# Performance work log

Hardware: AMD Instinct MI355X
Metric: run time of the kernel (lower is better)

## Reference

```python
import jax, jax.numpy as jnp
import numpy as np

SLOPE = 25.0  # snntorch surrogate.fast_sigmoid default slope

@jax.custom_vjp
def fast_sigmoid(x):
    # Forward: Heaviside step (spike); backward: fast-sigmoid surrogate grad.
    return (x > 0).astype(x.dtype)

def _fs_fwd(x):
    return fast_sigmoid(x), x

def _fs_bwd(x, g):
    return (g / (SLOPE * jnp.abs(x) + 1.0) ** 2,)

fast_sigmoid.defvjp(_fs_fwd, _fs_bwd)


def setup_inputs() -> dict:
    key = jax.random.key(0)
    k0, k1, k2, k3, k4 = jax.random.split(key, 5)
    B, IN, OUT, T = 512, 512, 512, 64
    x = jax.random.normal(k0, (B, IN), jnp.float32)
    W = jax.random.normal(k1, (OUT, IN), jnp.float32) / np.sqrt(IN).astype(np.float32)
    b = jnp.zeros((OUT,), jnp.float32)
    # learnable scalars (0.0 in source init; small nonzero to exercise the P recurrence)
    alpha = jax.random.uniform(k2, (1,), jnp.float32) * 0.1
    eta = jax.random.uniform(k3, (1,), jnp.float32) * 0.01
    beta = jax.random.uniform(k4, (1,), jnp.float32) * 0.1
    P0 = jnp.zeros((OUT, IN), jnp.float32)
    return {"x": x, "W": W, "b": b, "alpha": alpha, "eta": eta, "beta": beta, "P0": P0, "T": T}


def reference(x, W, b, alpha, eta, beta, P0, T):
    # x: [B, IN], W: [OUT, IN], P0: [OUT, IN]
    tao_u, tao_w, dt, V_th = 5.0, 1.0, 1.0, 0.2
    k = jnp.float32(dt / tao_u)
    a = alpha.reshape(())
    e = eta.reshape(())
    bt = beta.reshape(())
    # MLP output is constant across timesteps (same s_batch each step)
    mlp_T = jax.nn.relu(x @ W.T + b).T  # [OUT, B]
    xT = x.T  # [IN, B]
    decay_p = jnp.exp(jnp.float32(-dt / tao_w))

    # NOTE: reset() zeroes u and s every step, so only P is recurrent:
    # u_m = k * (mlp_out * exp(-m/tao_w) + alpha * P @ x^T)
    def step(P, m):
        u = k * (mlp_T * jnp.exp(-m / tao_w) + a * (P @ xT))  # [OUT, B]
        P_new = P * decay_p + e * ((fast_sigmoid(u) + bt) @ x)  # [OUT, IN]
        s = fast_sigmoid(u - V_th)  # [OUT, B]
        return P_new, s.T  # emit [B, OUT]

    _, spk = jax.lax.scan(step, P0, jnp.arange(T, dtype=jnp.float32))
    return spk  # [T, B, OUT]
```

## Files before the change

### kernel.cpp

```cpp
#include <hip/hip_runtime.h>


#define NN 512

__global__ __launch_bounds__(256) void gemm64_kernel(
    const float* __restrict__ x, const float* __restrict__ W,
    const float* __restrict__ P0, const float* __restrict__ bias,
    float* __restrict__ M, float* __restrict__ V0, float* __restrict__ G)
{
    const int tid = threadIdx.x;
    const int bid = blockIdx.x;
    const int out = bid >> 6;
    const int tl = bid & 63;
    const int rb = (tl >> 3) << 6;
    const int cb = (tl & 7) << 6;

    const float* A = ((out == 0) ? W : (out == 1) ? P0 : x) + (size_t)rb * NN;
    const float* Bx = x + (size_t)cb * NN;
    float* D = (out == 0) ? M : (out == 1) ? V0 : G;

    const int tx = tid & 15;
    const int ty = tid >> 4;

    __shared__ float At[32][68];
    __shared__ float Bt[32][68];

    const int lr = tid >> 2;
    const int lk = (tid & 3) << 3;

    float acc[4][4] = {{0.f,0.f,0.f,0.f},{0.f,0.f,0.f,0.f},
                       {0.f,0.f,0.f,0.f},{0.f,0.f,0.f,0.f}};

    float4 a0 = *(const float4*)(A + (size_t)lr * NN + lk);
    float4 a1 = *(const float4*)(A + (size_t)lr * NN + lk + 4);
    float4 b0 = *(const float4*)(Bx + (size_t)lr * NN + lk);
    float4 b1 = *(const float4*)(Bx + (size_t)lr * NN + lk + 4);

    for (int c = 0; c < 16; ++c) {
        __syncthreads();
        At[lk + 0][lr] = a0.x; At[lk + 1][lr] = a0.y;
        At[lk + 2][lr] = a0.z; At[lk + 3][lr] = a0.w;
        At[lk + 4][lr] = a1.x; At[lk + 5][lr] = a1.y;
        At[lk + 6][lr] = a1.z; At[lk + 7][lr] = a1.w;
        Bt[lk + 0][lr] = b0.x; Bt[lk + 1][lr] = b0.y;
        Bt[lk + 2][lr] = b0.z; Bt[lk + 3][lr] = b0.w;
        Bt[lk + 4][lr] = b1.x; Bt[lk + 5][lr] = b1.y;
        Bt[lk + 6][lr] = b1.z; Bt[lk + 7][lr] = b1.w;
        __syncthreads();

        if (c < 15) {
            const int k0 = (c + 1) << 5;
            a0 = *(const float4*)(A + (size_t)lr * NN + k0 + lk);
            a1 = *(const float4*)(A + (size_t)lr * NN + k0 + lk + 4);
            b0 = *(const float4*)(Bx + (size_t)lr * NN + k0 + lk);
            b1 = *(const float4*)(Bx + (size_t)lr * NN + k0 + lk + 4);
        }

#pragma unroll
        for (int k = 0; k < 32; ++k) {
            const float4 av = *(const float4*)&At[k][4 * ty];
            const float4 bv = *(const float4*)&Bt[k][4 * tx];
            const float avs[4] = {av.x, av.y, av.z, av.w};
            const float bvs[4] = {bv.x, bv.y, bv.z, bv.w};
#pragma unroll
            for (int i = 0; i < 4; ++i)
#pragma unroll
                for (int j = 0; j < 4; ++j)
                    acc[i][j] = fmaf(avs[i], bvs[j], acc[i][j]);
        }
    }

#pragma unroll
    for (int i = 0; i < 4; ++i) {
        const int r = rb + 4 * ty + i;
        float4 o = make_float4(acc[i][0], acc[i][1], acc[i][2], acc[i][3]);
        if (out == 0) {
            const float bb = bias[r];
            o.x = fmaxf(o.x + bb, 0.f); o.y = fmaxf(o.y + bb, 0.f);
            o.z = fmaxf(o.z + bb, 0.f); o.w = fmaxf(o.w + bb, 0.f);
        }
        *(float4*)(D + (size_t)r * NN + cb + 4 * tx) = o;
    }
}

__global__ __launch_bounds__(256) void acc0_kernel(
    const float* __restrict__ M, const float* __restrict__ V0,
    const float* __restrict__ G, const float* __restrict__ alpha,
    float* __restrict__ ACC0)
{
    const int tid = threadIdx.x;
    const int rb = (blockIdx.x >> 4) << 5;
    const int cb = (blockIdx.x & 15) << 5;
    const float a = alpha[0];
    const float kk = 0.2f;

    __shared__ float Ht[32][36];
    __shared__ float Bt[32][36];

    const int tx = tid & 15;
    const int ty = tid >> 4;
    const int lr = tid >> 3;
    const int lk = (tid & 7) << 2;

    float acc[2][2] = {{0.f, 0.f}, {0.f, 0.f}};

    for (int k0 = 0; k0 < NN; k0 += 32) {
        const float4 mv = *(const float4*)(M + (size_t)(rb + lr) * NN + k0 + lk);
        const float4 vv = *(const float4*)(V0 + (size_t)(rb + lr) * NN + k0 + lk);
        const float4 gv = *(const float4*)(G + (size_t)(k0 + lr) * NN + cb + lk);
        __syncthreads();
        Ht[lk + 0][lr] = (kk * fmaf(a, vv.x, mv.x) > 0.f) ? 1.f : 0.f;
        Ht[lk + 1][lr] = (kk * fmaf(a, vv.y, mv.y) > 0.f) ? 1.f : 0.f;
        Ht[lk + 2][lr] = (kk * fmaf(a, vv.z, mv.z) > 0.f) ? 1.f : 0.f;
        Ht[lk + 3][lr] = (kk * fmaf(a, vv.w, mv.w) > 0.f) ? 1.f : 0.f;
        Bt[lr][lk + 0] = gv.x; Bt[lr][lk + 1] = gv.y;
        Bt[lr][lk + 2] = gv.z; Bt[lr][lk + 3] = gv.w;
        __syncthreads();

#pragma unroll
        for (int k = 0; k < 32; ++k) {
            const float2 av = *(const float2*)&Ht[k][2 * ty];
            const float2 bv = *(const float2*)&Bt[k][2 * tx];
            acc[0][0] = fmaf(av.x, bv.x, acc[0][0]);
            acc[0][1] = fmaf(av.x, bv.y, acc[0][1]);
            acc[1][0] = fmaf(av.y, bv.x, acc[1][0]);
            acc[1][1] = fmaf(av.y, bv.y, acc[1][1]);
        }
    }

#pragma unroll
    for (int i = 0; i < 2; ++i) {
        *(float2*)(ACC0 + (size_t)(rb + 2 * ty + i) * NN + cb + 2 * tx) =
            make_float2(acc[i][0], acc[i][1]);
    }
}

__global__ __launch_bounds__(256) void colsum_kernel(
    const float* __restrict__ G, float* __restrict__ gs)
{
    __shared__ float red[4][64];
    const int tid = threadIdx.x;
    const int c = (blockIdx.x << 6) + (tid & 63);
    const int g = tid >> 6;
    float s = 0.f;
#pragma unroll 8
    for (int bp = 128 * g; bp < 128 * g + 128; ++bp) s += G[(size_t)bp * NN + c];
    if (g > 0) red[g][tid & 63] = s;
    __syncthreads();
    if (g == 0) gs[c] = ((s + red[1][tid & 63]) + red[2][tid & 63]) + red[3][tid & 63];
}

__global__ __launch_bounds__(512, 4) void snn_bits7_kernel(
    const float* __restrict__ M, const float* __restrict__ G,
    const float* __restrict__ V0, const float* __restrict__ ACC0,
    const float* __restrict__ gs, const float* __restrict__ alpha,
    const float* __restrict__ eta, const float* __restrict__ beta,
    unsigned* __restrict__ sp, int T)
{
    const int tid = threadIdx.x;
    const int w = tid >> 6;
    const int lane = tid & 63;
    const int r = blockIdx.x;

    __shared__ unsigned long long lflag[2];
    __shared__ int wcnt[8];
    __shared__ unsigned short list[528] __attribute__((aligned(16)));

    const float a = alpha[0], e = eta[0], bt = beta[0];
    const float kk = 0.2f;
    const float dd = 0.36787944117144233f;
    const float Vth = 0.2f;

    const size_t rc = (size_t)r * NN + tid;
    const float m = M[rc];
    float v = V0[rc];
    const float cg = e * bt * gs[tid];
    const float* Gc = G + tid;

    float acc;
    float em;
    unsigned long long oldw;

    {
        const float u = kk * fmaf(a, v, m * 1.0f);
        const unsigned long long hb = __ballot(u > 0.f);
        const unsigned long long sb = __ballot(u > Vth);
        if (lane == 0)
            *(unsigned long long*)(sp + (size_t)r * 16 + 2 * w) = sb;
        oldw = hb;
        acc = ACC0[rc];
        v = fmaf(dd, v, fmaf(e, acc, cg));
        em = dd;
    }

    for (int t = 1; t < T; ++t) {
        const float u = kk * fmaf(a, v, m * em);
        const unsigned long long hb = __ballot(u > 0.f);
        const unsigned long long sb = __ballot(u > Vth);
        const unsigned long long xw = hb ^ oldw;
        const int p = t & 1;
        if (lane == 0) {
            ((unsigned char*)&lflag[p])[w] = (xw != 0ull) ? (unsigned char)1 : (unsigned char)0;
            wcnt[w] = (int)__popcll(xw);
            *(unsigned long long*)(sp + ((size_t)t * NN + r) * 16 + 2 * w) = sb;
        }
        __syncthreads();

        if (lflag[p] != 0ull) {
            const int c0 = wcnt[0], c1 = wcnt[1], c2 = wcnt[2], c3 = wcnt[3];
            const int c4 = wcnt[4], c5 = wcnt[5], c6 = wcnt[6], c7 = wcnt[7];
            const int ntot = ((c0 + c1) + (c2 + c3)) + ((c4 + c5) + (c6 + c7));
            int base = 0;
            if (w > 0) base += c0;
            if (w > 1) base += c1;
            if (w > 2) base += c2;
            if (w > 3) base += c3;
            if (w > 4) base += c4;
            if (w > 5) base += c5;
            if (w > 6) base += c6;

            if ((xw >> lane) & 1ull) {
                const int pos = (int)__popcll(xw & ((1ull << lane) - 1ull));
                const unsigned row = (unsigned)((w << 6) + lane);
                const unsigned sgn = (unsigned)((hb >> lane) & 1ull) << 15;
                list[base + pos] = (unsigned short)(row | sgn);
            }
            __syncthreads();

            float s0 = 0.f, s1 = 0.f, s2 = 0.f, s3 = 0.f;
            float s4 = 0.f, s5 = 0.f, s6 = 0.f, s7 = 0.f;
            for (int j = 0; j < ntot; j += 8) {
                const uint4 le = *(const uint4*)(list + j);
                const unsigned e0 = le.x & 0xFFFFu, e1 = le.x >> 16;
                const unsigned e2 = le.y & 0xFFFFu, e3 = le.y >> 16;
                const unsigned e4 = le.z & 0xFFFFu, e5 = le.z >> 16;
                const unsigned e6 = le.w & 0xFFFFu, e7 = le.w >> 16;
                const float g0 = Gc[(size_t)(e0 & 511u) << 9];
                const float g1 = Gc[(size_t)(e1 & 511u) << 9];
                const float g2 = Gc[(size_t)(e2 & 511u) << 9];
                const float g3 = Gc[(size_t)(e3 & 511u) << 9];
                const float g4 = Gc[(size_t)(e4 & 511u) << 9];
                const float g5 = Gc[(size_t)(e5 & 511u) << 9];
                const float g6 = Gc[(size_t)(e6 & 511u) << 9];
                const float g7 = Gc[(size_t)(e7 & 511u) << 9];
                s0 += (j + 0 < ntot) ? ((e0 & 0x8000u) ? g0 : -g0) : 0.0f;
                s1 += (j + 1 < ntot) ? ((e1 & 0x8000u) ? g1 : -g1) : 0.0f;
                s2 += (j + 2 < ntot) ? ((e2 & 0x8000u) ? g2 : -g2) : 0.0f;
                s3 += (j + 3 < ntot) ? ((e3 & 0x8000u) ? g3 : -g3) : 0.0f;
                s4 += (j + 4 < ntot) ? ((e4 & 0x8000u) ? g4 : -g4) : 0.0f;
                s5 += (j + 5 < ntot) ? ((e5 & 0x8000u) ? g5 : -g5) : 0.0f;
                s6 += (j + 6 < ntot) ? ((e6 & 0x8000u) ? g6 : -g6) : 0.0f;
                s7 += (j + 7 < ntot) ? ((e7 & 0x8000u) ? g7 : -g7) : 0.0f;
            }
            acc += ((s0 + s1) + (s2 + s3)) + ((s4 + s5) + (s6 + s7));
        }

        oldw = hb;
        v = fmaf(dd, v, fmaf(e, acc, cg));
        em *= dd;
    }
}

__global__ __launch_bounds__(256) void expand_kernel(
    const unsigned* __restrict__ sp, float* __restrict__ out)
{
    const int tid = threadIdx.x;
    const int t = blockIdx.x >> 3;
    const int bt8 = blockIdx.x & 7;

    __shared__ uint2 sh[NN];
    const uint2* spw = (const uint2*)sp;
    sh[tid]       = spw[((size_t)t * NN + tid) * 8 + bt8];
    sh[tid + 256] = spw[((size_t)t * NN + tid + 256) * 8 + bt8];
    __syncthreads();

    const int b = bt8 * 64 + (tid >> 2);
    const int sub = tid & 3;
    const int rw = (tid >> 2) >> 5;
    const int bit = b & 31;
    float* op = out + (size_t)t * (NN * NN) + (size_t)b * NN;

#pragma unroll 4
    for (int i = 0; i < 32; ++i) {
        const int o = sub * 4 + i * 16;
        const uint2 w0 = sh[o];
        const uint2 w1 = sh[o + 1];
        const uint2 w2 = sh[o + 2];
        const uint2 w3 = sh[o + 3];
        float4 f;
        f.x = (float)(((rw ? w0.y : w0.x) >> bit) & 1u);
        f.y = (float)(((rw ? w1.y : w1.x) >> bit) & 1u);
        f.z = (float)(((rw ? w2.y : w2.x) >> bit) & 1u);
        f.w = (float)(((rw ? w3.y : w3.x) >> bit) & 1u);
        *(float4*)(op + o) = f;
    }
}

__global__ __launch_bounds__(256) void snn_step_kernel(
    const float* __restrict__ M, const float* __restrict__ G,
    const float* __restrict__ V0, const float* __restrict__ gs,
    const float* __restrict__ alpha, const float* __restrict__ eta,
    const float* __restrict__ beta, float* __restrict__ out, int T)
{
    const int j = threadIdx.x;
    const int r0 = blockIdx.x * 2;
    const int c0 = 2 * j;
    const float a = alpha[0], e = eta[0], bt = beta[0];
    const float kk = 0.2f, dd = 0.36787944117144233f, Vth = 0.2f;

    float v00 = V0[r0 * NN + c0];
    float v01 = V0[r0 * NN + c0 + 1];
    float v10 = V0[(r0 + 1) * NN + c0];
    float v11 = V0[(r0 + 1) * NN + c0 + 1];
    const float m00 = M[r0 * NN + c0];
    const float m01 = M[r0 * NN + c0 + 1];
    const float m10 = M[(r0 + 1) * NN + c0];
    const float m11 = M[(r0 + 1) * NN + c0 + 1];
    const float gs0 = gs[c0];
    const float gs1 = gs[c0 + 1];

    __shared__ float2 hp[NN];
    float em = 1.0f;
    const float2* Gcol = (const float2*)G + j;

    for (int t = 0; t < T; ++t) {
        const float u00 = kk * (m00 * em + a * v00);
        const float u01 = kk * (m01 * em + a * v01);
        const float u10 = kk * (m10 * em + a * v10);
        const float u11 = kk * (m11 * em + a * v11);

        float* outp = out + (size_t)t * (NN * NN);
        float2 sA = make_float2(u00 > Vth ? 1.f : 0.f, u10 > Vth ? 1.f : 0.f);
        float2 sB = make_float2(u01 > Vth ? 1.f : 0.f, u11 > Vth ? 1.f : 0.f);
        *(float2*)(outp + (size_t)c0 * NN + r0) = sA;
        *(float2*)(outp + (size_t)(c0 + 1) * NN + r0) = sB;

        hp[c0]     = make_float2(u00 > 0.f ? 1.f : 0.f, u10 > 0.f ? 1.f : 0.f);
        hp[c0 + 1] = make_float2(u01 > 0.f ? 1.f : 0.f, u11 > 0.f ? 1.f : 0.f);
        __syncthreads();

        float acc00 = 0.f, acc01 = 0.f, acc10 = 0.f, acc11 = 0.f;
#pragma unroll 8
        for (int bp = 0; bp < NN; ++bp) {
            float2 h = hp[bp];
            float2 g = Gcol[(size_t)bp * 256];
            acc00 = fmaf(h.x, g.x, acc00);
            acc01 = fmaf(h.x, g.y, acc01);
            acc10 = fmaf(h.y, g.x, acc10);
            acc11 = fmaf(h.y, g.y, acc11);
        }

        v00 = dd * v00 + e * (acc00 + bt * gs0);
        v01 = dd * v01 + e * (acc01 + bt * gs1);
        v10 = dd * v10 + e * (acc10 + bt * gs0);
        v11 = dd * v11 + e * (acc11 + bt * gs1);
        em *= dd;
        __syncthreads();
    }
}

extern "C" void kernel_launch(void* const* d_in, const int* in_sizes, int n_in,
                              void* d_out, int out_size, void* d_ws, size_t ws_size,
                              hipStream_t stream)
{
    const float* x     = (const float*)d_in[0];
    const float* W     = (const float*)d_in[1];
    const float* bias  = (const float*)d_in[2];
    const float* alpha = (const float*)d_in[3];
    const float* eta   = (const float*)d_in[4];
    const float* beta  = (const float*)d_in[5];
    const float* P0    = (const float*)d_in[6];
    (void)in_sizes; (void)n_in;

    const int T = out_size / (NN * NN);

    float* ws   = (float*)d_ws;
    float* M    = ws;
    float* V0   = ws + NN * NN;
    float* G    = ws + 2 * NN * NN;
    float* ACC0 = ws + 3 * NN * NN;
    float* gsv  = ws + 4 * NN * NN;
    unsigned* sp = (unsigned*)(gsv + NN);

    const size_t need_main = ((size_t)4 * NN * NN + NN) * 4 + (size_t)T * NN * 16 * 4;

    hipLaunchKernelGGL(gemm64_kernel, dim3(192), dim3(256), 0, stream,
                       x, W, P0, bias, M, V0, G);
    hipLaunchKernelGGL(colsum_kernel, dim3(8), dim3(256), 0, stream, G, gsv);

    if (ws_size >= need_main) {
        hipLaunchKernelGGL(acc0_kernel, dim3(256), dim3(256), 0, stream,
                           M, V0, G, alpha, ACC0);
        hipLaunchKernelGGL(snn_bits7_kernel, dim3(NN), dim3(512), 0, stream,
                           M, G, V0, ACC0, gsv, alpha, eta, beta, sp, T);
        hipLaunchKernelGGL(expand_kernel, dim3(T * 8), dim3(256), 0, stream,
                           sp, (float*)d_out);
    } else {
        hipLaunchKernelGGL(snn_step_kernel, dim3(256), dim3(256), 0, stream,
                           M, G, V0, gsv, alpha, eta, beta, (float*)d_out, T);
    }
}
```

Measured before the change: 131.2 us.

## Split-K the initial GEMMs, fuse column sum into ACC0 kernel, unroll gather by 16

The three 512x512 GEMMs are split four ways along K, going from 192 to 768 blocks so the GPU is better filled. A new combine kernel sums the partials and applies bias and ReLU. The column sum of G moves into the ACC0 kernel to save a launch, and the sparse gather loop in the main SNN kernel now processes 16 list entries per iteration to expose more memory-level parallelism. This costs an extra 12 matrices of workspace and extra global traffic for the partials. The original path is kept as a fallback when workspace is small.

```diff
diff --git a/kernel.cpp b/kernel.cpp
--- a/kernel.cpp
+++ b/kernel.cpp
@@ -3,21 +3,23 @@
 
 #define NN 512
 
-__global__ __launch_bounds__(256) void gemm64_kernel(
+__global__ __launch_bounds__(256) void gemm_splitk_kernel(
     const float* __restrict__ x, const float* __restrict__ W,
-    const float* __restrict__ P0, const float* __restrict__ bias,
-    float* __restrict__ M, float* __restrict__ V0, float* __restrict__ G)
+    const float* __restrict__ P0, float* __restrict__ part)
 {
     const int tid = threadIdx.x;
     const int bid = blockIdx.x;
-    const int out = bid >> 6;
-    const int tl = bid & 63;
+    const int out = bid >> 8;
+    const int rem = bid & 255;
+    const int kq = rem >> 6;
+    const int tl = rem & 63;
     const int rb = (tl >> 3) << 6;
     const int cb = (tl & 7) << 6;
+    const int kbase = kq << 7;
 
     const float* A = ((out == 0) ? W : (out == 1) ? P0 : x) + (size_t)rb * NN;
     const float* Bx = x + (size_t)cb * NN;
-    float* D = (out == 0) ? M : (out == 1) ? V0 : G;
+    float* D = part + (size_t)(out * 4 + kq) * NN * NN;
 
     const int tx = tid & 15;
     const int ty = tid >> 4;
@@ -31,12 +33,12 @@
     float acc[4][4] = {{0.f,0.f,0.f,0.f},{0.f,0.f,0.f,0.f},
                        {0.f,0.f,0.f,0.f},{0.f,0.f,0.f,0.f}};
 
-    float4 a0 = *(const float4*)(A + (size_t)lr * NN + lk);
-    float4 a1 = *(const float4*)(A + (size_t)lr * NN + lk + 4);
-    float4 b0 = *(const float4*)(Bx + (size_t)lr * NN + lk);
-    float4 b1 = *(const float4*)(Bx + (size_t)lr * NN + lk + 4);
-
-    for (int c = 0; c < 16; ++c) {
+    float4 a0 = *(const float4*)(A + (size_t)lr * NN + kbase + lk);
+    float4 a1 = *(const float4*)(A + (size_t)lr * NN + kbase + lk + 4);
+    float4 b0 = *(const float4*)(Bx + (size_t)lr * NN + kbase + lk);
+    float4 b1 = *(const float4*)(Bx + (size_t)lr * NN + kbase + lk + 4);
+
+    for (int c = 0; c < 4; ++c) {
         __syncthreads();
         At[lk + 0][lr] = a0.x; At[lk + 1][lr] = a0.y;
         At[lk + 2][lr] = a0.z; At[lk + 3][lr] = a0.w;
@@ -48,8 +50,8 @@
         Bt[lk + 6][lr] = b1.z; Bt[lk + 7][lr] = b1.w;
         __syncthreads();
 
-        if (c < 15) {
-            const int k0 = (c + 1) << 5;
+        if (c < 3) {
+            const int k0 = kbase + ((c + 1) << 5);
             a0 = *(const float4*)(A + (size_t)lr * NN + k0 + lk);
             a1 = *(const float4*)(A + (size_t)lr * NN + k0 + lk + 4);
             b0 = *(const float4*)(Bx + (size_t)lr * NN + k0 + lk);
@@ -73,20 +75,44 @@
 #pragma unroll
     for (int i = 0; i < 4; ++i) {
         const int r = rb + 4 * ty + i;
-        float4 o = make_float4(acc[i][0], acc[i][1], acc[i][2], acc[i][3]);
-        if (out == 0) {
-            const float bb = bias[r];
-            o.x = fmaxf(o.x + bb, 0.f); o.y = fmaxf(o.y + bb, 0.f);
-            o.z = fmaxf(o.z + bb, 0.f); o.w = fmaxf(o.w + bb, 0.f);
-        }
-        *(float4*)(D + (size_t)r * NN + cb + 4 * tx) = o;
-    }
-}
-
-__global__ __launch_bounds__(256) void acc0_kernel(
+        *(float4*)(D + (size_t)r * NN + cb + 4 * tx) =
+            make_float4(acc[i][0], acc[i][1], acc[i][2], acc[i][3]);
+    }
+}
+
+__global__ __launch_bounds__(256) void combine_kernel(
+    const float* __restrict__ part, const float* __restrict__ bias,
+    float* __restrict__ M, float* __restrict__ V0, float* __restrict__ G)
+{
+    const int idx = blockIdx.x * 256 + threadIdx.x;
+    const int out = idx >> 16;
+    const int io = idx & 65535;
+    const float4* p = (const float4*)(part + (size_t)out * 4 * NN * NN);
+    const float4 p0 = p[io];
+    const float4 p1 = p[io + 65536];
+    const float4 p2 = p[io + 131072];
+    const float4 p3 = p[io + 196608];
+    float4 s;
+    s.x = (p0.x + p1.x) + (p2.x + p3.x);
+    s.y = (p0.y + p1.y) + (p2.y + p3.y);
+    s.z = (p0.z + p1.z) + (p2.z + p3.z);
+    s.w = (p0.w + p1.w) + (p2.w + p3.w);
+    if (out == 0) {
+        const float bb = bias[io >> 7];
+        s.x = fmaxf(s.x + bb, 0.f); s.y = fmaxf(s.y + bb, 0.f);
+        s.z = fmaxf(s.z + bb, 0.f); s.w = fmaxf(s.w + bb, 0.f);
+        ((float4*)M)[io] = s;
+    } else if (out == 1) {
+        ((float4*)V0)[io] = s;
+    } else {
+        ((float4*)G)[io] = s;
+    }
+}
+
+__global__ __launch_bounds__(256) void acc0cs_kernel(
     const float* __restrict__ M, const float* __restrict__ V0,
     const float* __restrict__ G, const float* __restrict__ alpha,
-    float* __restrict__ ACC0)
+    float* __restrict__ ACC0, float* __restrict__ gs)
 {
     const int tid = threadIdx.x;
     const int rb = (blockIdx.x >> 4) << 5;
@@ -133,24 +159,29 @@
         *(float2*)(ACC0 + (size_t)(rb + 2 * ty + i) * NN + cb + 2 * tx) =
             make_float2(acc[i][0], acc[i][1]);
     }
-}
-
-__global__ __launch_bounds__(256) void colsum_kernel(
-    const float* __restrict__ G, float* __restrict__ gs)
-{
-    __shared__ float red[4][64];
-    const int tid = threadIdx.x;
-    const int c = (blockIdx.x << 6) + (tid & 63);
-    const int g = tid >> 6;
-    float s = 0.f;
+
+    if (rb == 0) {
+        __syncthreads();
+        float* red = (float*)Ht;
+        const int c = cb + (tid & 31);
+        const int g = tid >> 5;
+        float s = 0.f;
 #pragma unroll 8
-    for (int bp = 128 * g; bp < 128 * g + 128; ++bp) s += G[(size_t)bp * NN + c];
-    if (g > 0) red[g][tid & 63] = s;
-    __syncthreads();
-    if (g == 0) gs[c] = ((s + red[1][tid & 63]) + red[2][tid & 63]) + red[3][tid & 63];
-}
-
-__global__ __launch_bounds__(512, 4) void snn_bits7_kernel(
+        for (int bp = 64 * g; bp < 64 * g + 64; ++bp)
+            s += G[(size_t)bp * NN + c];
+        red[g * 32 + (tid & 31)] = s;
+        __syncthreads();
+        if (g == 0) {
+            const int cc = tid & 31;
+            const float tot =
+                ((red[cc] + red[32 + cc]) + (red[64 + cc] + red[96 + cc])) +
+                ((red[128 + cc] + red[160 + cc]) + (red[192 + cc] + red[224 + cc]));
+            gs[c] = tot;
+        }
+    }
+}
+
+__global__ __launch_bounds__(512, 4) void snn_bits8_kernel(
     const float* __restrict__ M, const float* __restrict__ G,
     const float* __restrict__ V0, const float* __restrict__ ACC0,
     const float* __restrict__ gs, const float* __restrict__ alpha,
@@ -164,7 +195,7 @@
 
     __shared__ unsigned long long lflag[2];
     __shared__ int wcnt[8];
-    __shared__ unsigned short list[528] __attribute__((aligned(16)));
+    __shared__ unsigned short list[544] __attribute__((aligned(16)));
 
     const float a = alpha[0], e = eta[0], bt = beta[0];
     const float kk = 0.2f;
@@ -229,12 +260,17 @@
 
             float s0 = 0.f, s1 = 0.f, s2 = 0.f, s3 = 0.f;
             float s4 = 0.f, s5 = 0.f, s6 = 0.f, s7 = 0.f;
-            for (int j = 0; j < ntot; j += 8) {
-                const uint4 le = *(const uint4*)(list + j);
-                const unsigned e0 = le.x & 0xFFFFu, e1 = le.x >> 16;
-                const unsigned e2 = le.y & 0xFFFFu, e3 = le.y >> 16;
-                const unsigned e4 = le.z & 0xFFFFu, e5 = le.z >> 16;
-                const unsigned e6 = le.w & 0xFFFFu, e7 = le.w >> 16;
+            for (int j = 0; j < ntot; j += 16) {
+                const uint4 leA = *(const uint4*)(list + j);
+                const uint4 leB = *(const uint4*)(list + j + 8);
+                const unsigned e0 = leA.x & 0xFFFFu,  e1 = leA.x >> 16;
+                const unsigned e2 = leA.y & 0xFFFFu,  e3 = leA.y >> 16;
+                const unsigned e4 = leA.z & 0xFFFFu,  e5 = leA.z >> 16;
+                const unsigned e6 = leA.w & 0xFFFFu,  e7 = leA.w >> 16;
+                const unsigned e8 = leB.x & 0xFFFFu,  e9 = leB.x >> 16;
+                const unsigned ea = leB.y & 0xFFFFu,  eb = leB.y >> 16;
+                const unsigned ec = leB.z & 0xFFFFu,  ed = leB.z >> 16;
+                const unsigned ee = leB.w & 0xFFFFu,  ef = leB.w >> 16;
                 const float g0 = Gc[(size_t)(e0 & 511u) << 9];
                 const float g1 = Gc[(size_t)(e1 & 511u) << 9];
                 const float g2 = Gc[(size_t)(e2 & 511u) << 9];
@@ -243,14 +279,30 @@
                 const float g5 = Gc[(size_t)(e5 & 511u) << 9];
                 const float g6 = Gc[(size_t)(e6 & 511u) << 9];
                 const float g7 = Gc[(size_t)(e7 & 511u) << 9];
-                s0 += (j + 0 < ntot) ? ((e0 & 0x8000u) ? g0 : -g0) : 0.0f;
-                s1 += (j + 1 < ntot) ? ((e1 & 0x8000u) ? g1 : -g1) : 0.0f;
-                s2 += (j + 2 < ntot) ? ((e2 & 0x8000u) ? g2 : -g2) : 0.0f;
-                s3 += (j + 3 < ntot) ? ((e3 & 0x8000u) ? g3 : -g3) : 0.0f;
-                s4 += (j + 4 < ntot) ? ((e4 & 0x8000u) ? g4 : -g4) : 0.0f;
-                s5 += (j + 5 < ntot) ? ((e5 & 0x8000u) ? g5 : -g5) : 0.0f;
-                s6 += (j + 6 < ntot) ? ((e6 & 0x8000u) ? g6 : -g6) : 0.0f;
-                s7 += (j + 7 < ntot) ? ((e7 & 0x8000u) ? g7 : -g7) : 0.0f;
+                const float g8 = Gc[(size_t)(e8 & 511u) << 9];
+                const float g9 = Gc[(size_t)(e9 & 511u) << 9];
+                const float ga = Gc[(size_t)(ea & 511u) << 9];
+                const float gb = Gc[(size_t)(eb & 511u) << 9];
+                const float gc2 = Gc[(size_t)(ec & 511u) << 9];
+                const float gd = Gc[(size_t)(ed & 511u) << 9];
+                const float ge = Gc[(size_t)(ee & 511u) << 9];
+                const float gf = Gc[(size_t)(ef & 511u) << 9];
+                s0 += (j + 0  < ntot) ? ((e0 & 0x8000u) ? g0 : -g0) : 0.0f;
+                s1 += (j + 1  < ntot) ? ((e1 & 0x8000u) ? g1 : -g1) : 0.0f;
+                s2 += (j + 2  < ntot) ? ((e2 & 0x8000u) ? g2 : -g2) : 0.0f;
+                s3 += (j + 3  < ntot) ? ((e3 & 0x8000u) ? g3 : -g3) : 0.0f;
+                s4 += (j + 4  < ntot) ? ((e4 & 0x8000u) ? g4 : -g4) : 0.0f;
+                s5 += (j + 5  < ntot) ? ((e5 & 0x8000u) ? g5 : -g5) : 0.0f;
+                s6 += (j + 6  < ntot) ? ((e6 & 0x8000u) ? g6 : -g6) : 0.0f;
+                s7 += (j + 7  < ntot) ? ((e7 & 0x8000u) ? g7 : -g7) : 0.0f;
+                s0 += (j + 8  < ntot) ? ((e8 & 0x8000u) ? g8 : -g8) : 0.0f;
+                s1 += (j + 9  < ntot) ? ((e9 & 0x8000u) ? g9 : -g9) : 0.0f;
+                s2 += (j + 10 < ntot) ? ((ea & 0x8000u) ? ga : -ga) : 0.0f;
+                s3 += (j + 11 < ntot) ? ((eb & 0x8000u) ? gb : -gb) : 0.0f;
+                s4 += (j + 12 < ntot) ? ((ec & 0x8000u) ? gc2 : -gc2) : 0.0f;
+                s5 += (j + 13 < ntot) ? ((ed & 0x8000u) ? gd : -gd) : 0.0f;
+                s6 += (j + 14 < ntot) ? ((ee & 0x8000u) ? ge : -ge) : 0.0f;
+                s7 += (j + 15 < ntot) ? ((ef & 0x8000u) ? gf : -gf) : 0.0f;
             }
             acc += ((s0 + s1) + (s2 + s3)) + ((s4 + s5) + (s6 + s7));
         }
@@ -296,6 +348,101 @@
     }
 }
 
+__global__ __launch_bounds__(256) void gemm64_kernel(
+    const float* __restrict__ x, const float* __restrict__ W,
+    const float* __restrict__ P0, const float* __restrict__ bias,
+    float* __restrict__ M, float* __restrict__ V0, float* __restrict__ G)
+{
+    const int tid = threadIdx.x;
+    const int bid = blockIdx.x;
+    const int out = bid >> 6;
+    const int tl = bid & 63;
+    const int rb = (tl >> 3) << 6;
+    const int cb = (tl & 7) << 6;
+
+    const float* A = ((out == 0) ? W : (out == 1) ? P0 : x) + (size_t)rb * NN;
+    const float* Bx = x + (size_t)cb * NN;
+    float* D = (out == 0) ? M : (out == 1) ? V0 : G;
+
+    const int tx = tid & 15;
+    const int ty = tid >> 4;
+
+    __shared__ float At[32][68];
+    __shared__ float Bt[32][68];
+
+    const int lr = tid >> 2;
+    const int lk = (tid & 3) << 3;
+
+    float acc[4][4] = {{0.f,0.f,0.f,0.f},{0.f,0.f,0.f,0.f},
+                       {0.f,0.f,0.f,0.f},{0.f,0.f,0.f,0.f}};
+
+    float4 a0 = *(const float4*)(A + (size_t)lr * NN + lk);
+    float4 a1 = *(const float4*)(A + (size_t)lr * NN + lk + 4);
+    float4 b0 = *(const float4*)(Bx + (size_t)lr * NN + lk);
+    float4 b1 = *(const float4*)(Bx + (size_t)lr * NN + lk + 4);
+
+    for (int c = 0; c < 16; ++c) {
+        __syncthreads();
+        At[lk + 0][lr] = a0.x; At[lk + 1][lr] = a0.y;
+        At[lk + 2][lr] = a0.z; At[lk + 3][lr] = a0.w;
+        At[lk + 4][lr] = a1.x; At[lk + 5][lr] = a1.y;
+        At[lk + 6][lr] = a1.z; At[lk + 7][lr] = a1.w;
+        Bt[lk + 0][lr] = b0.x; Bt[lk + 1][lr] = b0.y;
+        Bt[lk + 2][lr] = b0.z; Bt[lk + 3][lr] = b0.w;
+        Bt[lk + 4][lr] = b1.x; Bt[lk + 5][lr] = b1.y;
+        Bt[lk + 6][lr] = b1.z; Bt[lk + 7][lr] = b1.w;
+        __syncthreads();
+
+        if (c < 15) {
+            const int k0 = (c + 1) << 5;
+            a0 = *(const float4*)(A + (size_t)lr * NN + k0 + lk);
+            a1 = *(const float4*)(A + (size_t)lr * NN + k0 + lk + 4);
+            b0 = *(const float4*)(Bx + (size_t)lr * NN + k0 + lk);
+            b1 = *(const float4*)(Bx + (size_t)lr * NN + k0 + lk + 4);
+        }
+
+#pragma unroll
+        for (int k = 0; k < 32; ++k) {
+            const float4 av = *(const float4*)&At[k][4 * ty];
+            const float4 bv = *(const float4*)&Bt[k][4 * tx];
+            const float avs[4] = {av.x, av.y, av.z, av.w};
+            const float bvs[4] = {bv.x, bv.y, bv.z, bv.w};
+#pragma unroll
+            for (int i = 0; i < 4; ++i)
+#pragma unroll
+                for (int j = 0; j < 4; ++j)
+                    acc[i][j] = fmaf(avs[i], bvs[j], acc[i][j]);
+        }
+    }
+
+#pragma unroll
+    for (int i = 0; i < 4; ++i) {
+        const int r = rb + 4 * ty + i;
+        float4 o = make_float4(acc[i][0], acc[i][1], acc[i][2], acc[i][3]);
+        if (out == 0) {
+            const float bb = bias[r];
+            o.x = fmaxf(o.x + bb, 0.f); o.y = fmaxf(o.y + bb, 0.f);
+            o.z = fmaxf(o.z + bb, 0.f); o.w = fmaxf(o.w + bb, 0.f);
+        }
+        *(float4*)(D + (size_t)r * NN + cb + 4 * tx) = o;
+    }
+}
+
+__global__ __launch_bounds__(256) void colsum_kernel(
+    const float* __restrict__ G, float* __restrict__ gs)
+{
+    __shared__ float red[4][64];
+    const int tid = threadIdx.x;
+    const int c = (blockIdx.x << 6) + (tid & 63);
+    const int g = tid >> 6;
+    float s = 0.f;
+#pragma unroll 8
+    for (int bp = 128 * g; bp < 128 * g + 128; ++bp) s += G[(size_t)bp * NN + c];
+    if (g > 0) red[g][tid & 63] = s;
+    __syncthreads();
+    if (g == 0) gs[c] = ((s + red[1][tid & 63]) + red[2][tid & 63]) + red[3][tid & 63];
+}
+
 __global__ __launch_bounds__(256) void snn_step_kernel(
     const float* __restrict__ M, const float* __restrict__ G,
     const float* __restrict__ V0, const float* __restrict__ gs,
@@ -375,28 +522,36 @@
     const int T = out_size / (NN * NN);
 
     float* ws   = (float*)d_ws;
-    float* M    = ws;
-    float* V0   = ws + NN * NN;
-    float* G    = ws + 2 * NN * NN;
-    float* ACC0 = ws + 3 * NN * NN;
-    float* gsv  = ws + 4 * NN * NN;
+    float* part = ws;
+    float* M    = ws + 12 * NN * NN;
+    float* V0   = ws + 13 * NN * NN;
+    float* G    = ws + 14 * NN * NN;
+    float* ACC0 = ws + 15 * NN * NN;
+    float* gsv  = ws + 16 * NN * NN;
     unsigned* sp = (unsigned*)(gsv + NN);
 
-    const size_t need_main = ((size_t)4 * NN * NN + NN) * 4 + (size_t)T * NN * 16 * 4;
-
-    hipLaunchKernelGGL(gemm64_kernel, dim3(192), dim3(256), 0, stream,
-                       x, W, P0, bias, M, V0, G);
-    hipLaunchKernelGGL(colsum_kernel, dim3(8), dim3(256), 0, stream, G, gsv);
+    const size_t need_main = ((size_t)16 * NN * NN + NN) * 4 + (size_t)T * NN * 16 * 4;
 
     if (ws_size >= need_main) {
-        hipLaunchKernelGGL(acc0_kernel, dim3(256), dim3(256), 0, stream,
-                           M, V0, G, alpha, ACC0);
-        hipLaunchKernelGGL(snn_bits7_kernel, dim3(NN), dim3(512), 0, stream,
+        hipLaunchKernelGGL(gemm_splitk_kernel, dim3(768), dim3(256), 0, stream,
+                           x, W, P0, part);
+        hipLaunchKernelGGL(combine_kernel, dim3(768), dim3(256), 0, stream,
+                           part, bias, M, V0, G);
+        hipLaunchKernelGGL(acc0cs_kernel, dim3(256), dim3(256), 0, stream,
+                           M, V0, G, alpha, ACC0, gsv);
+        hipLaunchKernelGGL(snn_bits8_kernel, dim3(NN), dim3(512), 0, stream,
                            M, G, V0, ACC0, gsv, alpha, eta, beta, sp, T);
         hipLaunchKernelGGL(expand_kernel, dim3(T * 8), dim3(256), 0, stream,
                            sp, (float*)d_out);
     } else {
+        float* Mf  = ws;
+        float* V0f = ws + NN * NN;
+        float* Gf  = ws + 2 * NN * NN;
+        float* gs2 = ws + 3 * NN * NN;
+        hipLaunchKernelGGL(gemm64_kernel, dim3(192), dim3(256), 0, stream,
+                           x, W, P0, bias, Mf, V0f, Gf);
+        hipLaunchKernelGGL(colsum_kernel, dim3(8), dim3(256), 0, stream, Gf, gs2);
         hipLaunchKernelGGL(snn_step_kernel, dim3(256), dim3(256), 0, stream,
-                           M, G, V0, gsv, alpha, eta, beta, (float*)d_out, T);
-    }
-}
+                           Mf, Gf, V0f, gs2, alpha, eta, beta, (float*)d_out, T);
+    }
+}
```

Measured after the change: 126.9 us. 1.03x faster.
